# Optimization experiments

Hardware: AMD Instinct MI355X
Metric: run time of the kernel (lower is better)

Reference implementation:

```python
import jax, jax.numpy as jnp
import numpy as np

RADIUS = 1.0
NSAMPLE = 32


def setup_inputs() -> dict:
    key = jax.random.key(0)
    k1, k2, k3, k4, k5 = jax.random.split(key, 5)
    B, Nb, M, K, C = 2, 2048, 64, 216, 32
    N = B * Nb
    # points in a 20m cube
    xyz = jax.random.uniform(k1, (N, 3), dtype=jnp.float32) * 20.0
    xyz_batch_cnt = jnp.array([Nb, Nb], dtype=jnp.int32)
    # rois: [x,y,z,dx,dy,dz,ry]
    ctr = jax.random.uniform(k2, (B, M, 3), dtype=jnp.float32) * 20.0
    dims = 1.0 + jax.random.uniform(k3, (B, M, 3), dtype=jnp.float32) * 2.0
    ry = jax.random.uniform(k4, (B, M, 1), dtype=jnp.float32) * 6.28
    rois = jnp.concatenate([ctr, dims, ry], axis=-1)
    # 6x6x6 grid points jittered around each roi center
    off = (jax.random.uniform(k5, (B, M, K, 3), dtype=jnp.float32) - 0.5) * 3.0
    new_xyz = ctr[:, :, None, :] + off
    features = jax.random.normal(jax.random.fold_in(key, 7), (N, C), dtype=jnp.float32)
    return {"xyz": xyz, "xyz_batch_cnt": xyz_batch_cnt, "new_xyz": new_xyz,
            "rois": rois, "features": features}


def _query_and_group(xyz, new_xyz, rois, features, B, Nb):
    """Ball query -> ragged compaction (padded to L=N*nsample) -> gather."""
    M, K = new_xyz.shape[1], new_xyz.shape[2]
    MK = M * K
    N = B * Nb
    L = N * NSAMPLE
    xyz_b = xyz.reshape(B, Nb, 3)
    grid = new_xyz.reshape(B, MK, 3)
    # squared distances point -> grid center, (B, Nb, MK)
    d2 = jnp.sum((xyz_b[:, :, None, :] - grid[:, None, :, :]) ** 2, axis=-1)
    # roi bounding sphere: center rois[:,:,:3], radius ||dims||_2 (the `ball` tensor)
    ctr = rois[:, :, :3]
    r2 = jnp.sum(rois[:, :, 3:6] ** 2, axis=-1)          # (B, M)
    d2b = jnp.sum((xyz_b[:, :, None, :] - ctr[:, None, :, :]) ** 2, axis=-1)  # (B,Nb,M)
    in_ball = (d2b <= r2[:, None, :])[:, :, :, None]      # (B,Nb,M,1)
    mask = (d2 <= RADIUS * RADIUS) & jnp.broadcast_to(in_ball, (B, Nb, M, K)).reshape(B, Nb, MK)
    # first-NSAMPLE-in-order selection per point (matches kernel iteration order)
    rank = jnp.cumsum(mask.astype(jnp.int32), axis=2) - 1
    cols = jnp.where(mask & (rank < NSAMPLE), rank, NSAMPLE)  # NSAMPLE = OOB -> dropped
    rows = jnp.broadcast_to(
        jnp.arange(B, dtype=jnp.int32)[:, None, None] * Nb
        + jnp.arange(Nb, dtype=jnp.int32)[None, :, None], (B, Nb, MK))
    flat_idx = jnp.broadcast_to(
        jnp.arange(B, dtype=jnp.int32)[:, None, None] * MK
        + jnp.arange(MK, dtype=jnp.int32)[None, None, :], (B, Nb, MK))
    ball_idx = jnp.full((N, NSAMPLE), -1, dtype=jnp.int32)
    ball_idx = ball_idx.at[rows.reshape(-1), cols.reshape(-1)].set(
        flat_idx.reshape(-1), mode="drop")
    # BallIndice: cumsum compaction of valid (point_idx, grid_idx) pairs, row-major
    valid = (ball_idx > -1).reshape(-1)                  # (L,)
    pos = jnp.cumsum(valid.astype(jnp.int32)) - 1
    pos_w = jnp.where(valid, pos, L)                     # invalid -> OOB -> dropped
    row_ids = jnp.broadcast_to(
        jnp.arange(N, dtype=jnp.int32)[:, None], (N, NSAMPLE)).reshape(-1)
    set_indices = jnp.zeros((L,), jnp.int32).at[pos_w].set(row_ids, mode="drop")
    set_new_indices = jnp.zeros((L,), jnp.int32).at[pos_w].set(
        ball_idx.reshape(-1), mode="drop")
    nind = jnp.sum(valid.astype(jnp.int32))
    vm = (jnp.arange(L) < nind)[:, None].astype(features.dtype)  # padding mask
    # GatherFeature (padded slots zeroed, matching new_zeros semantics)
    group_xyz = xyz[set_indices] * vm
    group_new_xyz = new_xyz.reshape(-1, 3)[set_new_indices] * vm
    group_feat = features[set_indices] * vm
    group_features = jnp.concatenate([group_xyz - group_new_xyz, group_feat], axis=1)
    return group_features, set_new_indices


def reference(xyz, xyz_batch_cnt, new_xyz, rois, features):
    B = xyz_batch_cnt.shape[0]
    Nb = xyz.shape[0] // B
    return _query_and_group(xyz, new_xyz, rois, features, B, Nb)
```

## Files before the change

kernel.cpp:

```cpp
#include <hip/hip_runtime.h>


#pragma clang fp contract(off)

typedef unsigned long long u64;
typedef float f32x4 __attribute__((ext_vector_type(4)));

#define MAXN 4096
#define RPB 8

template <typename IT>
__global__ __launch_bounds__(512) void count_kernel(
    const float* __restrict__ xyz, const float* __restrict__ new_xyz,
    const float* __restrict__ rois, int* __restrict__ counts,
    int* __restrict__ blockSums, IT* __restrict__ ballidx,
    int N, int Nb, int M, int K, int nsample)
{
    __shared__ int plist[RPB][64];
    __shared__ int scnt[RPB];
    const int wave = threadIdx.x >> 6;
    const int lane = threadIdx.x & 63;
    const int r = blockIdx.x * RPB + wave;
    const u64 laneLt = (1ull << lane) - 1ull;

    int cntc = 0;
    if (r < N) {
        const int b  = r / Nb;
        const float px = xyz[3 * r + 0];
        const float py = xyz[3 * r + 1];
        const float pz = xyz[3 * r + 2];

        bool pass = false;
        if (lane < M) {
            const float* rp = rois + (size_t)(b * M + lane) * 7;
            const float dx = rp[3], dy = rp[4], dz = rp[5];
            const float r2 = (dx * dx + dy * dy) + dz * dz;
            const float ex = px - rp[0], ey = py - rp[1], ez = pz - rp[2];
            pass = ((ex * ex + ey * ey) + ez * ez) <= r2;
        }
        const u64 roiMask = __ballot(pass);
        if (roiMask) {
            if (pass) plist[wave][__popcll(roiMask & laneLt)] = lane;

            const int P = __popcll(roiMask);
            const int total = P * K;
            const float* nb_ = new_xyz + (size_t)(b * M * K) * 3;
            IT* bi = ballidx + (size_t)r * nsample;

            int cnt = 0;
            for (int base = 0; base < total && cnt < nsample; base += 512) {
                bool match[8];
                int jj[8];
                #pragma unroll
                for (int u = 0; u < 8; u++) {
                    const int p = base + u * 64 + lane;
                    match[u] = false; jj[u] = 0;
                    if (p < total) {
                        const int ri = p / K;
                        const int k  = p - ri * K;
                        const int j  = plist[wave][ri] * K + k;
                        jj[u] = j;
                        const float* gp = nb_ + (size_t)j * 3;
                        const float ax = px - gp[0], ay = py - gp[1], az = pz - gp[2];
                        match[u] = ((ax * ax + ay * ay) + az * az) <= 1.0f;
                    }
                }
                #pragma unroll
                for (int u = 0; u < 8; u++) {
                    const u64 mm = __ballot(match[u]);
                    const int slot = cnt + __popcll(mm & laneLt);
                    if (match[u] && slot < nsample) bi[slot] = (IT)jj[u];
                    cnt += __popcll(mm);
                }
            }
            cntc = cnt > nsample ? nsample : cnt;
        }
        if (lane == 0) counts[r] = cntc;
    }
    if (lane == 0) scnt[wave] = cntc;
    __syncthreads();
    if (threadIdx.x == 0) {
        int s = 0;
        #pragma unroll
        for (int i = 0; i < RPB; i++) s += scnt[i];
        blockSums[blockIdx.x] = s;
    }
}

template <typename IT>
__global__ __launch_bounds__(512) void emit_kernel(
    const float* __restrict__ xyz, const float* __restrict__ new_xyz,
    const float* __restrict__ features,
    const int* __restrict__ counts, const int* __restrict__ blockSums,
    const IT* __restrict__ ballidx,
    float* __restrict__ out_feat, float* __restrict__ out_idx,
    int N, int Nb, int M, int K, int C, int nsample, int numBlocks)
{
    const int t = threadIdx.x;
    const int lane = t & 63;
    const int wid = t >> 6;
    const int bid = blockIdx.x;

    int pre = 0, tot = 0;
    {
        const int g = (lane + bid) & 63;
        for (int idx = g; idx < numBlocks; idx += 64) {
            const int v = blockSums[idx];
            tot += v;
            if (idx < bid) pre += v;
        }
        #pragma unroll
        for (int d = 1; d < 64; d <<= 1) {
            pre += __shfl_xor(pre, d, 64);
            tot += __shfl_xor(tot, d, 64);
        }
    }
    const int blockPre = pre;
    const int nind     = tot;

    const int W = 3 + C;
    const size_t L = (size_t)N * nsample;
    const int r0 = bid * RPB;
    const int r  = r0 + wid;

    if (r < N) {
        const int cnt = counts[r];
        if (cnt > 0) {
            int rowpre = 0;
            if (lane < wid && (r0 + lane) < N) rowpre = counts[r0 + lane];
            #pragma unroll
            for (int d = 1; d < 64; d <<= 1) rowpre += __shfl_xor(rowpre, d, 64);

            const int b  = r / Nb;
            const int MK = M * K;
            const int obase = blockPre + rowpre;
            const IT* bi = ballidx + (size_t)r * nsample;
            const float px = xyz[3 * r + 0];
            const float py = xyz[3 * r + 1];
            const float pz = xyz[3 * r + 2];
            const float* fr = features + (size_t)r * C;
            const float* nb_ = new_xyz + (size_t)b * MK * 3;

            float* dst = out_feat + (size_t)obase * W;
            const int totE = cnt * W;
            for (int idx = lane; idx < totE; idx += 64) {
                const int s = idx / W;
                const int c = idx - s * W;
                const int j = (int)bi[s];
                float v;
                if (c == 0)      v = px - nb_[(size_t)j * 3 + 0];
                else if (c == 1) v = py - nb_[(size_t)j * 3 + 1];
                else if (c == 2) v = pz - nb_[(size_t)j * 3 + 2];
                else             v = fr[c - 3];
                __builtin_nontemporal_store(v, &dst[idx]);
            }
            for (int s = lane; s < cnt; s += 64)
                __builtin_nontemporal_store((float)(b * MK + (int)bi[s]),
                                            &out_idx[obase + s]);
        }
    }

    const int gtid = bid * 512 + t;
    const size_t gthreads = (size_t)numBlocks * 512;
    {
        const size_t sA = (size_t)nind * W;
        const size_t eA = L * (size_t)W;
        if (sA < eA) {
            const size_t s4 = (sA + 3) & ~(size_t)3;
            const size_t headEnd = s4 < eA ? s4 : eA;
            if ((size_t)gtid < headEnd - sA)
                __builtin_nontemporal_store(0.0f, &out_feat[sA + gtid]);
            if (s4 < eA) {
                const size_t nvec = (eA - s4) >> 2;
                f32x4* p4 = (f32x4*)(out_feat + s4);
                const f32x4 z = {0.0f, 0.0f, 0.0f, 0.0f};
                for (size_t i = gtid; i < nvec; i += gthreads)
                    __builtin_nontemporal_store(z, &p4[i]);
                const size_t rem = (eA - s4) & 3;
                if ((size_t)gtid < rem)
                    __builtin_nontemporal_store(0.0f, &out_feat[eA - rem + gtid]);
            }
        }
    }
    for (size_t i = (size_t)nind + gtid; i < L; i += gthreads)
        __builtin_nontemporal_store(0.0f, &out_idx[i]);
}

extern "C" void kernel_launch(void* const* d_in, const int* in_sizes, int n_in,
                              void* d_out, int out_size, void* d_ws, size_t ws_size,
                              hipStream_t stream) {
    if (n_in < 5) return;

    int bc = 0;
    for (int i = 1; i < n_in; i++) if (in_sizes[i] < in_sizes[bc]) bc = i;
    const int B = in_sizes[bc];
    if (B < 1) return;

    int xi = -1, nwi = -1, ri = -1, fi = -1;
    int N = 0, M = 0, K = 0, C = 0, nsample = 0;

    for (int rr = 0; rr < n_in && xi < 0; rr++) {
        if (rr == bc) continue;
        if (in_sizes[rr] % (7 * B)) continue;
        const int M_ = in_sizes[rr] / (7 * B);
        if (M_ < 1 || M_ > 64) continue;
        for (int xx = 0; xx < n_in && xi < 0; xx++) {
            if (xx == bc || xx == rr) continue;
            if (in_sizes[xx] % 3) continue;
            const int N_ = in_sizes[xx] / 3;
            if (N_ < B || N_ % B || N_ > MAXN) continue;
            for (int nn = 0; nn < n_in && xi < 0; nn++) {
                if (nn == bc || nn == rr || nn == xx) continue;
                if (in_sizes[nn] % (3 * B * M_)) continue;
                const int K_ = in_sizes[nn] / (3 * B * M_);
                if (K_ < 1) continue;
                for (int ff = 0; ff < n_in && xi < 0; ff++) {
                    if (ff == bc || ff == rr || ff == xx || ff == nn) continue;
                    if (in_sizes[ff] % N_) continue;
                    const int C_ = in_sizes[ff] / N_;
                    if (C_ < 1) continue;
                    if (out_size % (4 + C_)) continue;
                    const long long L_ = (long long)out_size / (4 + C_);
                    if (L_ % N_) continue;
                    const int ns = (int)(L_ / N_);
                    if (ns < 1 || ns > 1024) continue;
                    xi = xx; nwi = nn; ri = rr; fi = ff;
                    N = N_; M = M_; K = K_; C = C_; nsample = ns;
                }
            }
        }
    }
    if (xi < 0) return;

    const float* xyz      = (const float*)d_in[xi];
    const float* new_xyz  = (const float*)d_in[nwi];
    const float* rois     = (const float*)d_in[ri];
    const float* features = (const float*)d_in[fi];
    const int Nb = N / B;

    const size_t L      = (size_t)N * nsample;
    const size_t chunk0 = L * (size_t)(3 + C);

    float* out_feat = (float*)d_out;
    float* out_idx  = out_feat + chunk0;

    const int blocks = (N + RPB - 1) / RPB;

    const size_t wsNeed = ((size_t)N + (size_t)blocks + (size_t)N * nsample) * sizeof(int);
    if (ws_size < wsNeed) return;
    int* counts    = (int*)d_ws;
    int* blockSums = counts + N;
    void* ballidx  = (void*)(blockSums + blocks);

    const bool idx16 = ((long long)M * K <= 65535);

    if (idx16) {
        count_kernel<unsigned short><<<blocks, 512, 0, stream>>>(
            xyz, new_xyz, rois, counts, blockSums, (unsigned short*)ballidx,
            N, Nb, M, K, nsample);
        emit_kernel<unsigned short><<<blocks, 512, 0, stream>>>(
            xyz, new_xyz, features, counts, blockSums, (const unsigned short*)ballidx,
            out_feat, out_idx, N, Nb, M, K, C, nsample, blocks);
    } else {
        count_kernel<int><<<blocks, 512, 0, stream>>>(
            xyz, new_xyz, rois, counts, blockSums, (int*)ballidx,
            N, Nb, M, K, nsample);
        emit_kernel<int><<<blocks, 512, 0, stream>>>(
            xyz, new_xyz, features, counts, blockSums, (const int*)ballidx,
            out_feat, out_idx, N, Nb, M, K, C, nsample, blocks);
    }
}
```

Before: 90.41 us.

## Zero full output in count kernel, slim emit kernel, halve block size

Moves zero-filling of the entire padded output (features and indices) into the count kernel, so the emit kernel only writes valid rows and early-exits for empty rows. The emit kernel now computes just its prefix, with no global total, and uses regular stores instead of nontemporal ones. Rows per block drop from 8 to 4 with 256-thread blocks, and the p/K division is replaced by a magic-number multiply. This rewrites the output region twice for valid rows, relying on stream ordering. It also adds a memset for any tail that does not fill a full vector.

```diff
diff --git a/kernel.cpp b/kernel.cpp
--- a/kernel.cpp
+++ b/kernel.cpp
@@ -7,14 +7,15 @@
 typedef float f32x4 __attribute__((ext_vector_type(4)));
 
 #define MAXN 4096
-#define RPB 8
+#define RPB 4
 
 template <typename IT>
-__global__ __launch_bounds__(512) void count_kernel(
+__global__ __launch_bounds__(256) void count_kernel(
     const float* __restrict__ xyz, const float* __restrict__ new_xyz,
     const float* __restrict__ rois, int* __restrict__ counts,
     int* __restrict__ blockSums, IT* __restrict__ ballidx,
-    int N, int Nb, int M, int K, int nsample)
+    float* __restrict__ out_all,
+    int N, int Nb, int M, int K, int nsample, unsigned magicK, int nOutVec4)
 {
     __shared__ int plist[RPB][64];
     __shared__ int scnt[RPB];
@@ -22,6 +23,15 @@
     const int lane = threadIdx.x & 63;
     const int r = blockIdx.x * RPB + wave;
     const u64 laneLt = (1ull << lane) - 1ull;
+
+    {
+        const int gtid = blockIdx.x * 256 + threadIdx.x;
+        const int gthreads = gridDim.x * 256;
+        f32x4* p4 = (f32x4*)out_all;
+        const f32x4 z = {0.0f, 0.0f, 0.0f, 0.0f};
+        for (int i = gtid; i < nOutVec4; i += gthreads)
+            __builtin_nontemporal_store(z, &p4[i]);
+    }
 
     int cntc = 0;
     if (r < N) {
@@ -56,7 +66,7 @@
                     const int p = base + u * 64 + lane;
                     match[u] = false; jj[u] = 0;
                     if (p < total) {
-                        const int ri = p / K;
+                        const int ri = (int)(((u64)(unsigned)p * magicK) >> 32);
                         const int k  = p - ri * K;
                         const int j  = plist[wave][ri] * K + k;
                         jj[u] = j;
@@ -88,7 +98,7 @@
 }
 
 template <typename IT>
-__global__ __launch_bounds__(512) void emit_kernel(
+__global__ __launch_bounds__(256) void emit_kernel(
     const float* __restrict__ xyz, const float* __restrict__ new_xyz,
     const float* __restrict__ features,
     const int* __restrict__ counts, const int* __restrict__ blockSums,
@@ -101,89 +111,51 @@
     const int wid = t >> 6;
     const int bid = blockIdx.x;
 
-    int pre = 0, tot = 0;
-    {
-        const int g = (lane + bid) & 63;
-        for (int idx = g; idx < numBlocks; idx += 64) {
-            const int v = blockSums[idx];
-            tot += v;
-            if (idx < bid) pre += v;
-        }
-        #pragma unroll
-        for (int d = 1; d < 64; d <<= 1) {
-            pre += __shfl_xor(pre, d, 64);
-            tot += __shfl_xor(tot, d, 64);
-        }
-    }
-    const int blockPre = pre;
-    const int nind     = tot;
-
-    const int W = 3 + C;
-    const size_t L = (size_t)N * nsample;
     const int r0 = bid * RPB;
     const int r  = r0 + wid;
-
-    if (r < N) {
-        const int cnt = counts[r];
-        if (cnt > 0) {
-            int rowpre = 0;
-            if (lane < wid && (r0 + lane) < N) rowpre = counts[r0 + lane];
-            #pragma unroll
-            for (int d = 1; d < 64; d <<= 1) rowpre += __shfl_xor(rowpre, d, 64);
-
-            const int b  = r / Nb;
-            const int MK = M * K;
-            const int obase = blockPre + rowpre;
-            const IT* bi = ballidx + (size_t)r * nsample;
-            const float px = xyz[3 * r + 0];
-            const float py = xyz[3 * r + 1];
-            const float pz = xyz[3 * r + 2];
-            const float* fr = features + (size_t)r * C;
-            const float* nb_ = new_xyz + (size_t)b * MK * 3;
-
-            float* dst = out_feat + (size_t)obase * W;
-            const int totE = cnt * W;
-            for (int idx = lane; idx < totE; idx += 64) {
-                const int s = idx / W;
-                const int c = idx - s * W;
-                const int j = (int)bi[s];
-                float v;
-                if (c == 0)      v = px - nb_[(size_t)j * 3 + 0];
-                else if (c == 1) v = py - nb_[(size_t)j * 3 + 1];
-                else if (c == 2) v = pz - nb_[(size_t)j * 3 + 2];
-                else             v = fr[c - 3];
-                __builtin_nontemporal_store(v, &dst[idx]);
-            }
-            for (int s = lane; s < cnt; s += 64)
-                __builtin_nontemporal_store((float)(b * MK + (int)bi[s]),
-                                            &out_idx[obase + s]);
-        }
-    }
-
-    const int gtid = bid * 512 + t;
-    const size_t gthreads = (size_t)numBlocks * 512;
-    {
-        const size_t sA = (size_t)nind * W;
-        const size_t eA = L * (size_t)W;
-        if (sA < eA) {
-            const size_t s4 = (sA + 3) & ~(size_t)3;
-            const size_t headEnd = s4 < eA ? s4 : eA;
-            if ((size_t)gtid < headEnd - sA)
-                __builtin_nontemporal_store(0.0f, &out_feat[sA + gtid]);
-            if (s4 < eA) {
-                const size_t nvec = (eA - s4) >> 2;
-                f32x4* p4 = (f32x4*)(out_feat + s4);
-                const f32x4 z = {0.0f, 0.0f, 0.0f, 0.0f};
-                for (size_t i = gtid; i < nvec; i += gthreads)
-                    __builtin_nontemporal_store(z, &p4[i]);
-                const size_t rem = (eA - s4) & 3;
-                if ((size_t)gtid < rem)
-                    __builtin_nontemporal_store(0.0f, &out_feat[eA - rem + gtid]);
-            }
-        }
-    }
-    for (size_t i = (size_t)nind + gtid; i < L; i += gthreads)
-        __builtin_nontemporal_store(0.0f, &out_idx[i]);
+    if (r >= N) return;
+    const int cnt = counts[r];
+    if (cnt <= 0) return;
+
+    int pre = 0;
+    if (bid > 0) {
+        const int g = (lane + bid) & 63;
+        for (int idx = g; idx < bid; idx += 64) pre += blockSums[idx];
+        #pragma unroll
+        for (int d = 1; d < 64; d <<= 1) pre += __shfl_xor(pre, d, 64);
+    }
+
+    int rowpre = 0;
+    if (lane < wid && (r0 + lane) < N) rowpre = counts[r0 + lane];
+    #pragma unroll
+    for (int d = 1; d < 64; d <<= 1) rowpre += __shfl_xor(rowpre, d, 64);
+
+    const int W = 3 + C;
+    const int b  = r / Nb;
+    const int MK = M * K;
+    const int obase = pre + rowpre;
+    const IT* bi = ballidx + (size_t)r * nsample;
+    const float px = xyz[3 * r + 0];
+    const float py = xyz[3 * r + 1];
+    const float pz = xyz[3 * r + 2];
+    const float* fr = features + (size_t)r * C;
+    const float* nb_ = new_xyz + (size_t)b * MK * 3;
+
+    float* dst = out_feat + (size_t)obase * W;
+    const int totE = cnt * W;
+    for (int idx = lane; idx < totE; idx += 64) {
+        const int s = idx / W;
+        const int c = idx - s * W;
+        const int j = (int)bi[s];
+        float v;
+        if (c == 0)      v = px - nb_[(size_t)j * 3 + 0];
+        else if (c == 1) v = py - nb_[(size_t)j * 3 + 1];
+        else if (c == 2) v = pz - nb_[(size_t)j * 3 + 2];
+        else             v = fr[c - 3];
+        dst[idx] = v;
+    }
+    for (int s = lane; s < cnt; s += 64)
+        out_idx[obase + s] = (float)(b * MK + (int)bi[s]);
 }
 
 extern "C" void kernel_launch(void* const* d_in, const int* in_sizes, int n_in,
@@ -240,6 +212,7 @@
 
     const size_t L      = (size_t)N * nsample;
     const size_t chunk0 = L * (size_t)(3 + C);
+    const size_t totalOut = chunk0 + L;
 
     float* out_feat = (float*)d_out;
     float* out_idx  = out_feat + chunk0;
@@ -252,21 +225,28 @@
     int* blockSums = counts + N;
     void* ballidx  = (void*)(blockSums + blocks);
 
+    const unsigned magicK = (unsigned)((0x100000000ULL + (u64)K - 1) / (u64)K);
+    const int nOutVec4 = (int)(totalOut >> 2);
     const bool idx16 = ((long long)M * K <= 65535);
 
     if (idx16) {
-        count_kernel<unsigned short><<<blocks, 512, 0, stream>>>(
+        count_kernel<unsigned short><<<blocks, 256, 0, stream>>>(
             xyz, new_xyz, rois, counts, blockSums, (unsigned short*)ballidx,
-            N, Nb, M, K, nsample);
-        emit_kernel<unsigned short><<<blocks, 512, 0, stream>>>(
+            (float*)d_out, N, Nb, M, K, nsample, magicK, nOutVec4);
+        emit_kernel<unsigned short><<<blocks, 256, 0, stream>>>(
             xyz, new_xyz, features, counts, blockSums, (const unsigned short*)ballidx,
             out_feat, out_idx, N, Nb, M, K, C, nsample, blocks);
     } else {
-        count_kernel<int><<<blocks, 512, 0, stream>>>(
+        count_kernel<int><<<blocks, 256, 0, stream>>>(
             xyz, new_xyz, rois, counts, blockSums, (int*)ballidx,
-            N, Nb, M, K, nsample);
-        emit_kernel<int><<<blocks, 512, 0, stream>>>(
+            (float*)d_out, N, Nb, M, K, nsample, magicK, nOutVec4);
+        emit_kernel<int><<<blocks, 256, 0, stream>>>(
             xyz, new_xyz, features, counts, blockSums, (const int*)ballidx,
             out_feat, out_idx, N, Nb, M, K, C, nsample, blocks);
     }
+
+    if (totalOut & 3) {
+        hipMemsetAsync((float*)d_out + (totalOut & ~(size_t)3), 0,
+                       (totalOut & 3) * sizeof(float), stream);
+    }
 }
```

Result: no change. 91.05 us (+0.7%).
